# Performance work log

Measured on AMD Instinct MI355X. Metric: run time of the kernel, lower is better.

## Reference

```python
import jax, jax.numpy as jnp
import numpy as np

V, E, H, B, S, T, FF = 50000, 128, 256, 32, 256, 32, 4096
START = 2  # tokenizer.word_index['<start>'] stand-in


def setup_inputs() -> dict:
    key = jax.random.key(0)
    ks = jax.random.split(key, 16)
    g = lambda k, shape, s=0.05: (jax.random.normal(k, shape) * s).astype(jnp.float32)
    z = lambda shape: jnp.zeros(shape, jnp.float32)
    return {
        "inp": jax.random.randint(ks[0], (B, S), 0, V, dtype=jnp.int32),
        "targ": jax.random.randint(ks[1], (B, T), 0, V, dtype=jnp.int32),
        "emb": g(ks[2], (V, E)),
        "ek_f": g(ks[3], (E, 4 * H)), "er_f": g(ks[4], (H, 4 * H)), "eb_f": z((4 * H,)),
        "ek_b": g(ks[5], (E, 4 * H)), "er_b": g(ks[6], (H, 4 * H)), "eb_b": z((4 * H,)),
        "dk": g(ks[7], (E, 4 * H)), "dr": g(ks[8], (H, 4 * H)), "db": z((4 * H,)),
        "henc_w": g(ks[9], (2 * H, E)), "henc_b": z((E,)),
        "sdec_w": g(ks[10], (H, E)), "sdec_b": z((E,)),
        "vatt": g(ks[11], (E, 1)),
        "lf_w": g(ks[12], (2 * H + H, FF), 0.02), "lf_b": z((FF,)),
        "lv_w": g(ks[13], (FF, V), 0.02), "lv_b": z((V,)),
    }


def _lstm_cell(x, h, c, k, rk, b):
    # Keras LSTM gate order: i, f, g(candidate), o
    zg = x @ k + h @ rk + b
    i, f, g, o = jnp.split(zg, 4, axis=-1)
    c = jax.nn.sigmoid(f) * c + jax.nn.sigmoid(i) * jnp.tanh(g)
    h = jax.nn.sigmoid(o) * jnp.tanh(c)
    return h, c


def _run_lstm(xs, k, rk, b):
    # xs: [S, B, E] -> outputs [S, B, H]
    h0 = jnp.zeros((xs.shape[1], rk.shape[0]), xs.dtype)

    def step(carry, x):
        h, c = _lstm_cell(x, carry[0], carry[1], k, rk, b)
        return (h, c), h

    _, hs = jax.lax.scan(step, (h0, h0), xs)
    return hs


def reference(inp, targ, emb, ek_f, er_f, eb_f, ek_b, er_b, eb_b, dk, dr, db,
              henc_w, henc_b, sdec_w, sdec_b, vatt, lf_w, lf_b, lv_w, lv_b):
    # ---- BiLSTM encoder ----
    xs = emb[inp].transpose(1, 0, 2)                       # [S, B, E]
    fwd = _run_lstm(xs, ek_f, er_f, eb_f)                  # [S, B, H]
    bwd = _run_lstm(xs[::-1], ek_b, er_b, eb_b)[::-1]      # [S, B, H]
    enc = jnp.concatenate([fwd, bwd], -1).transpose(1, 0, 2)  # [B, S, 2H]
    henc_proj = enc @ henc_w + henc_b                      # [B, S, E] (loop-invariant)

    # Teacher forcing: step t (t=1..T-1) consumes <start> then targ[:, t-1]
    tok_in = jnp.concatenate(
        [jnp.full((B, 1), START, targ.dtype), targ[:, 1:T - 1]], axis=1)  # [B, T-1]
    tgts = targ[:, 1:]                                     # [B, T-1]
    h0 = jnp.zeros((B, H), jnp.float32)

    def dec_step(carry, tt):
        h, c = carry
        tok, tgt = tt
        h, c = _lstm_cell(emb[tok], h, c, dk, dr, db)
        # Bahdanau attention (note: original uses carry c, not hidden h)
        scores = jnp.tanh(henc_proj + (c @ sdec_w + sdec_b)[:, None, :])  # [B, S, E]
        attn = jax.nn.softmax(scores @ vatt, axis=1)        # [B, S, 1]
        context = jnp.sum(enc * attn, axis=1)               # [B, 2H]
        combined = jnp.concatenate([context, c], axis=1)    # [B, 3H]
        logits = (combined @ lf_w + lf_b) @ lv_w + lv_b     # [B, V]
        logp = jax.nn.log_softmax(logits, axis=-1)
        nll = -jnp.take_along_axis(logp, tgt[:, None].astype(jnp.int32), axis=1)[:, 0]
        mask = (tgt != 0).astype(nll.dtype)
        return (h, c), jnp.mean(nll * mask)

    _, losses = jax.lax.scan(dec_step, (h0, h0), (tok_in.T, tgts.T))
    return jnp.sum(losses) / T
```

## Files before the change

kernel.cpp:

```cpp
#include <hip/hip_runtime.h>

#define DEV __device__ __forceinline__

typedef __attribute__((ext_vector_type(8))) short bf16x8;
typedef __attribute__((ext_vector_type(4))) float f32x4;
typedef __attribute__((ext_vector_type(2))) _Float16 h2_t;

typedef __attribute__((address_space(1))) const void GLDg;
typedef __attribute__((address_space(3))) void GLDl;

static const int V = 50000, E = 128, H = 256, B = 32, S = 256, T = 32, FF = 4096;
static const int NCT = 391;
static const int NPART = 782;
static const size_t OFF_XKF  = 0;
static const size_t OFF_XKB  = 8388608;
static const size_t OFF_XKD  = 16777216;
static const size_t OFF_HSF  = 17825792;
static const size_t OFF_HSB  = 19922944;
static const size_t OFF_HENC = 22020096;
static const size_t OFF_ERPF = 23068672;
static const size_t OFF_ERPB = 23199744;
static const size_t OFF_DRP  = 23330816;
static const size_t OFF_COMB = 23461888;
static const size_t OFF_FB16 = 23855104;
static const size_t OFF_LFWT = 25952256;
static const size_t OFF_LVWT = 27525120;
static const size_t LVWT_FLOATS = 102498304;
static const size_t WS_NEED_BYTES = (OFF_LVWT + LVWT_FLOATS) * 4;
static const size_t OFF_PMAX = 0;
static const size_t OFF_PSUM = 800768;
static const size_t OFF_TLOG = 1601536;
static const size_t OFF_NLL  = 1602560;
static const size_t OFF_CT   = 1603584;

static const size_t ENC_LDS_BYTES = 65536 * 2 + 512 + 4096;

DEV float sigf(float x) { return 1.0f / (1.0f + __expf(-x)); }
DEV float tanh_(float x) {
    x = fminf(fmaxf(x, -20.0f), 20.0f);
    float e = __expf(2.0f * x);
    return (e - 1.0f) / (e + 1.0f);
}
DEV unsigned short f2bf(float f) {
    unsigned int u = __builtin_bit_cast(unsigned int, f);
    u += 0x7FFFu + ((u >> 16) & 1u);
    return (unsigned short)(u >> 16);
}
DEV float bf2f(unsigned short s) {
    unsigned int u = ((unsigned int)s) << 16;
    return __builtin_bit_cast(float, u);
}
DEV float dot2u(unsigned int a, unsigned int b, float c) {
#if __has_builtin(__builtin_amdgcn_fdot2)
    return __builtin_amdgcn_fdot2(__builtin_bit_cast(h2_t, a), __builtin_bit_cast(h2_t, b), c, false);
#else
    h2_t x = __builtin_bit_cast(h2_t, a), y = __builtin_bit_cast(h2_t, b);
    return c + (float)x[0] * (float)y[0] + (float)x[1] * (float)y[1];
#endif
}

__global__ void pack_half_k(const float* __restrict__ erf, const float* __restrict__ erb,
                            const float* __restrict__ dr,
                            unsigned int* __restrict__ pf, unsigned int* __restrict__ pb,
                            unsigned int* __restrict__ pd) {
    int id = blockIdx.x * 256 + threadIdx.x;
    int which = id >> 17;
    int rem = id & 131071;
    const float* s = (which == 0) ? erf : (which == 1) ? erb : dr;
    unsigned int* o = (which == 0) ? pf : (which == 1) ? pb : pd;
    int cc = rem >> 7, k2 = rem & 127;
    float v0 = s[(2 * k2) * 1024 + cc];
    float v1 = s[(2 * k2 + 1) * 1024 + cc];
    h2_t h; h[0] = (_Float16)v0; h[1] = (_Float16)v1;
    o[rem] = __builtin_bit_cast(unsigned int, h);
}

__global__ __launch_bounds__(256) void xgate_kernel(const float* __restrict__ emb,
                                                    const int* __restrict__ tok_src, int dec_mode,
                                                    const float* __restrict__ wt,
                                                    const float* __restrict__ bias,
                                                    float* __restrict__ out) {
    __shared__ float Al[64][128];
    __shared__ int tk[64];
    int r0 = blockIdx.x * 64, c0b = blockIdx.y * 128;
    int tid = threadIdx.x;
    if (tid < 64) {
        int r = r0 + tid; int hi = r >> 5, b = r & 31; int token;
        if (dec_mode) token = (hi == 0) ? 2 : tok_src[b * 32 + hi];
        else          token = tok_src[b * 256 + hi];
        tk[tid] = token;
    }
    __syncthreads();
    {
        int ri = tid >> 2, cc = (tid & 3) * 32;
        const float4* src = (const float4*)&emb[(size_t)tk[ri] * 128 + cc];
        float4* dst = (float4*)&Al[ri][cc];
#pragma unroll
        for (int i = 0; i < 8; ++i) dst[i] = src[i];
    }
    __syncthreads();
    int rg = tid >> 5;
    int c = c0b + (tid & 31) * 4;
    float4 acc[8];
#pragma unroll
    for (int r = 0; r < 8; ++r) acc[r] = make_float4(0.f, 0.f, 0.f, 0.f);
    for (int k = 0; k < 128; k += 4) {
        float4 w0 = *(const float4*)&wt[(k + 0) * 1024 + c];
        float4 w1 = *(const float4*)&wt[(k + 1) * 1024 + c];
        float4 w2 = *(const float4*)&wt[(k + 2) * 1024 + c];
        float4 w3 = *(const float4*)&wt[(k + 3) * 1024 + c];
#pragma unroll
        for (int r = 0; r < 8; ++r) {
            float4 a = *(const float4*)&Al[rg * 8 + r][k];
            acc[r].x += a.x * w0.x + a.y * w1.x + a.z * w2.x + a.w * w3.x;
            acc[r].y += a.x * w0.y + a.y * w1.y + a.z * w2.y + a.w * w3.y;
            acc[r].z += a.x * w0.z + a.y * w1.z + a.z * w2.z + a.w * w3.z;
            acc[r].w += a.x * w0.w + a.y * w1.w + a.z * w2.w + a.w * w3.w;
        }
    }
    float4 b4 = *(const float4*)&bias[c];
#pragma unroll
    for (int r = 0; r < 8; ++r) {
        int row = r0 + rg * 8 + r;
        float4 v = make_float4(acc[r].x + b4.x, acc[r].y + b4.y, acc[r].z + b4.z, acc[r].w + b4.w);
        *(float4*)&out[(size_t)row * 1024 + c] = v;
    }
}

extern __shared__ unsigned char dyn_lds[];
__global__ __launch_bounds__(512)
__attribute__((amdgpu_waves_per_eu(2, 2)))
void lstm_cvt_fused(
        const float* __restrict__ xkf, const float* __restrict__ xkb,
        const unsigned int* __restrict__ erpf, const unsigned int* __restrict__ erpb,
        float* __restrict__ hsf, float* __restrict__ hsb,
        const float* __restrict__ xkd, const unsigned int* __restrict__ drp,
        float* __restrict__ ct_all, unsigned short* __restrict__ comb16,
        const float* __restrict__ lfw, unsigned short* __restrict__ lfwT,
        const float* __restrict__ lvw, unsigned short* __restrict__ lvwT) {
    int bid = blockIdx.x;
    int tid = threadIdx.x;
    if (bid < 96) {
        int is_dec = (bid >= 64);
        int dir = is_dec ? 0 : (bid >> 5);
        int row = is_dec ? (bid - 64) : (bid & 31);
        const float* xk = is_dec ? xkd : (dir ? xkb : xkf);
        const unsigned int* erp = is_dec ? drp : (dir ? erpb : erpf);
        float* hs = dir ? hsb : hsf;
        int nsteps = is_dec ? 31 : 256;
        int ca = 2 * tid;
        uint4* wlA = (uint4*)dyn_lds;
        uint4* wlB = (uint4*)(dyn_lds + 65536);
        unsigned int* h2 = (unsigned int*)(dyn_lds + 131072);
        float* zg = (float*)(dyn_lds + 131072 + 512);

        const uint4* pa = (const uint4*)&erp[(size_t)ca * 128];
        const uint4* pb = (const uint4*)&erp[(size_t)(ca + 1) * 128];
        uint4 wa[24], wb[24];
#pragma unroll
        for (int i = 0; i < 24; ++i) { wa[i] = pa[i]; wb[i] = pb[i]; }
#pragma unroll
        for (int i = 0; i < 24; ++i) {
            asm volatile("" : "+v"(wa[i].x), "+v"(wa[i].y), "+v"(wa[i].z), "+v"(wa[i].w),
                             "+v"(wb[i].x), "+v"(wb[i].y), "+v"(wb[i].z), "+v"(wb[i].w));
        }
#pragma unroll
        for (int j = 0; j < 8; ++j) { wlA[j * 512 + tid] = pa[24 + j]; wlB[j * 512 + tid] = pb[24 + j]; }
        if (tid < 128) h2[tid] = 0u;
        float c_reg = 0.0f;
        __syncthreads();
        int s0 = (!is_dec && dir) ? (nsteps - 1) : 0;
        float2 xcur = *(const float2*)&xk[(size_t)(s0 * 32 + row) * 1024 + ca];
        for (int si = 0; si < nsteps; ++si) {
            int s = (!is_dec && dir) ? (nsteps - 1 - si) : si;
            float2 xnext = make_float2(0.f, 0.f);
            if (si + 1 < nsteps) {
                int sn = (!is_dec && dir) ? (nsteps - 2 - si) : (si + 1);
                xnext = *(const float2*)&xk[(size_t)(sn * 32 + row) * 1024 + ca];
            }
            float acc0 = xcur.x, acc1 = xcur.y;
#pragma unroll
            for (int i = 0; i < 24; ++i) {
                uint4 hv = *(const uint4*)&h2[4 * i];
                acc0 = dot2u(hv.x, wa[i].x, acc0);
                acc0 = dot2u(hv.y, wa[i].y, acc0);
                acc0 = dot2u(hv.z, wa[i].z, acc0);
                acc0 = dot2u(hv.w, wa[i].w, acc0);
                acc1 = dot2u(hv.x, wb[i].x, acc1);
                acc1 = dot2u(hv.y, wb[i].y, acc1);
                acc1 = dot2u(hv.z, wb[i].z, acc1);
                acc1 = dot2u(hv.w, wb[i].w, acc1);
            }
#pragma unroll
            for (int j = 0; j < 8; ++j) {
                uint4 hv = *(const uint4*)&h2[96 + 4 * j];
                uint4 qa = wlA[j * 512 + tid];
                uint4 qb = wlB[j * 512 + tid];
                acc0 = dot2u(hv.x, qa.x, acc0);
                acc0 = dot2u(hv.y, qa.y, acc0);
                acc0 = dot2u(hv.z, qa.z, acc0);
                acc0 = dot2u(hv.w, qa.w, acc0);
                acc1 = dot2u(hv.x, qb.x, acc1);
                acc1 = dot2u(hv.y, qb.y, acc1);
                acc1 = dot2u(hv.z, qb.z, acc1);
                acc1 = dot2u(hv.w, qb.w, acc1);
            }
            *(float2*)&zg[ca] = make_float2(acc0, acc1);
            __syncthreads();
            if (tid < 256) {
                float ii = zg[tid], ff = zg[tid + 256], gg = zg[tid + 512], oo = zg[tid + 768];
                c_reg = sigf(ff) * c_reg + sigf(ii) * tanh_(gg);
                float h = sigf(oo) * tanh_(c_reg);
                ((_Float16*)h2)[tid] = (_Float16)h;
                if (is_dec) {
                    ct_all[(size_t)(s * 32 + row) * 256 + tid] = c_reg;
                    comb16[(size_t)(s * 32 + row) * 768 + 512 + tid] = f2bf(c_reg);
                } else {
                    hs[(size_t)(s * 32 + row) * 256 + tid] = h;
                }
            }
            __syncthreads();
            xcur = xnext;
        }
        if (is_dec) {
            size_t base = (size_t)(31 * 32 + row) * 768;
            for (int j = tid; j < 768; j += 512) comb16[base + j] = 0;
        }
    } else {
        const float* src; unsigned short* dst; int N, ldd, nb, kb, nmax;
        if (bid < 96 + 192) {
            int f2 = bid - 96;
            src = lfw; dst = lfwT; N = 4096; ldd = 768; nmax = 4096;
            nb = (f2 & 15) * 256; kb = (f2 >> 4) * 64;
        } else {
            int f3 = bid - 288;
            src = lvw; dst = lvwT; N = 50000; ldd = 4096; nmax = 50048;
            int nbi = f3 % 196, kbi = f3 / 196;
            nb = nbi * 256; kb = kbi * 64;
        }
        unsigned int* l32 = (unsigned int*)dyn_lds;
        int nl = tid & 63, kg = tid >> 6;
        float4 v[8];
        if (nb + 256 <= N) {
            const float* sp = src + (size_t)(kb + kg * 8) * N + nb + nl * 4;
#pragma unroll
            for (int j = 0; j < 8; ++j) v[j] = *(const float4*)(sp + (size_t)j * N);
        } else {
#pragma unroll
            for (int j = 0; j < 8; ++j) {
                int n0 = nb + nl * 4;
                const float* rp = src + (size_t)(kb + kg * 8 + j) * N;
                v[j].x = (n0 + 0 < N) ? rp[n0 + 0] : 0.0f;
                v[j].y = (n0 + 1 < N) ? rp[n0 + 1] : 0.0f;
                v[j].z = (n0 + 2 < N) ? rp[n0 + 2] : 0.0f;
                v[j].w = (n0 + 3 < N) ? rp[n0 + 3] : 0.0f;
            }
        }
#pragma unroll
        for (int p = 0; p < 4; ++p) {
            unsigned int d0 = (unsigned int)f2bf(v[2 * p].x) | ((unsigned int)f2bf(v[2 * p + 1].x) << 16);
            unsigned int d1 = (unsigned int)f2bf(v[2 * p].y) | ((unsigned int)f2bf(v[2 * p + 1].y) << 16);
            unsigned int d2 = (unsigned int)f2bf(v[2 * p].z) | ((unsigned int)f2bf(v[2 * p + 1].z) << 16);
            unsigned int d3 = (unsigned int)f2bf(v[2 * p].w) | ((unsigned int)f2bf(v[2 * p + 1].w) << 16);
            *(uint4*)&l32[(size_t)(kg * 4 + p) * 260 + nl * 4] = make_uint4(d0, d1, d2, d3);
        }
        __syncthreads();
#pragma unroll
        for (int i = 0; i < 4; ++i) {
            int cid = i * 512 + tid;
            int nloc = cid >> 3, kc = cid & 7;
            int n = nb + nloc;
            if (n < nmax) {
                unsigned int u0 = l32[(size_t)(kc * 4 + 0) * 260 + nloc];
                unsigned int u1 = l32[(size_t)(kc * 4 + 1) * 260 + nloc];
                unsigned int u2 = l32[(size_t)(kc * 4 + 2) * 260 + nloc];
                unsigned int u3 = l32[(size_t)(kc * 4 + 3) * 260 + nloc];
                *(uint4*)&dst[(size_t)n * ldd + kb + kc * 8] = make_uint4(u0, u1, u2, u3);
            }
        }
    }
}

__global__ __launch_bounds__(256) void dec_attn(const float* __restrict__ ct_all,
                                                const float* __restrict__ sdw, const float* __restrict__ sdb,
                                                const float* __restrict__ vatt,
                                                const float* __restrict__ henc,
                                                const float* __restrict__ hsf, const float* __restrict__ hsb,
                                                unsigned short* __restrict__ comb16) {
    int per = (int)gridDim.x >> 3;
    int f = ((int)blockIdx.x & 7) * per + ((int)blockIdx.x >> 3);
    int row = f / 31, t = f - row * 31;
    int tid = threadIdx.x;
    __shared__ float c_l[256];
    __shared__ float catt[128];
    __shared__ float attn[256];
    __shared__ float red[256];
    __shared__ float vat[128];
    __shared__ float part[256];
    c_l[tid] = ct_all[(size_t)(t * 32 + row) * 256 + tid];
    if (tid < 128) vat[tid] = vatt[tid];
    __syncthreads();
    {
        int col = tid & 127, k0 = (tid >> 7) * 128;
        float aa = 0.0f;
#pragma unroll 4
        for (int k = 0; k < 128; ++k) aa += c_l[k0 + k] * sdw[(size_t)(k0 + k) * 128 + col];
        part[tid] = aa;
    }
    __syncthreads();
    if (tid < 128) catt[tid] = part[tid] + part[tid + 128] + sdb[tid];
    __syncthreads();
    {
        const float4* hp = (const float4*)&henc[(size_t)(row * 256 + tid) * 128];
        float aa = 0.0f;
#pragma unroll 4
        for (int e4 = 0; e4 < 32; ++e4) {
            float4 h4 = hp[e4];
            int e = 4 * e4;
            aa += tanh_(h4.x + catt[e + 0]) * vat[e + 0];
            aa += tanh_(h4.y + catt[e + 1]) * vat[e + 1];
            aa += tanh_(h4.z + catt[e + 2]) * vat[e + 2];
            aa += tanh_(h4.w + catt[e + 3]) * vat[e + 3];
        }
        attn[tid] = aa;
    }
    __syncthreads();
    red[tid] = attn[tid];
    __syncthreads();
    for (int off = 128; off; off >>= 1) {
        if (tid < off) red[tid] = fmaxf(red[tid], red[tid + off]);
        __syncthreads();
    }
    float mx = red[0];
    __syncthreads();
    float ex = __expf(attn[tid] - mx);
    red[tid] = ex;
    __syncthreads();
    for (int off = 128; off; off >>= 1) {
        if (tid < off) red[tid] += red[tid + off];
        __syncthreads();
    }
    float inv = 1.0f / red[0];
    __syncthreads();
    attn[tid] = ex * inv;
    __syncthreads();
    {
        float cx0 = 0.0f, cx1 = 0.0f;
#pragma unroll 4
        for (int s = 0; s < 256; ++s) {
            float aw = attn[s];
            cx0 += aw * hsf[(size_t)(s * 32 + row) * 256 + tid];
            cx1 += aw * hsb[(size_t)(s * 32 + row) * 256 + tid];
        }
        size_t base = (size_t)(t * 32 + row) * 768;
        comb16[base + tid] = f2bf(cx0);
        comb16[base + 256 + tid] = f2bf(cx1);
    }
}

__global__ __launch_bounds__(256) void henc_kernel(const float* __restrict__ hsf, const float* __restrict__ hsb,
                                                   const float* __restrict__ hw, const float* __restrict__ hb,
                                                   float* __restrict__ henc) {
    __shared__ float Al[32][256];
    int r0 = blockIdx.x * 32;
    int tid = threadIdx.x;
    int rg = tid >> 5;
    int c = (tid & 31) * 4;
    float4 acc[4];
#pragma unroll
    for (int r = 0; r < 4; ++r) acc[r] = make_float4(0.f, 0.f, 0.f, 0.f);
    for (int kc = 0; kc < 2; ++kc) {
        const float* src_arr = kc ? hsb : hsf;
        {
            int ri = tid >> 3, cc = (tid & 7) * 32;
            int r = r0 + ri; int b = r >> 8, s = r & 255;
            const float4* sp = (const float4*)&src_arr[(size_t)(s * 32 + b) * 256 + cc];
            float4* dp = (float4*)&Al[ri][cc];
#pragma unroll
            for (int i = 0; i < 8; ++i) dp[i] = sp[i];
        }
        __syncthreads();
        for (int k = 0; k < 256; k += 4) {
            int kg = kc * 256 + k;
            float4 w0 = *(const float4*)&hw[(kg + 0) * 128 + c];
            float4 w1 = *(const float4*)&hw[(kg + 1) * 128 + c];
            float4 w2 = *(const float4*)&hw[(kg + 2) * 128 + c];
            float4 w3 = *(const float4*)&hw[(kg + 3) * 128 + c];
#pragma unroll
            for (int r = 0; r < 4; ++r) {
                float4 a = *(const float4*)&Al[rg * 4 + r][k];
                acc[r].x += a.x * w0.x + a.y * w1.x + a.z * w2.x + a.w * w3.x;
                acc[r].y += a.x * w0.y + a.y * w1.y + a.z * w2.y + a.w * w3.y;
                acc[r].z += a.x * w0.z + a.y * w1.z + a.z * w2.z + a.w * w3.z;
                acc[r].w += a.x * w0.w + a.y * w1.w + a.z * w2.w + a.w * w3.w;
            }
        }
        __syncthreads();
    }
    float4 b4 = *(const float4*)&hb[c];
#pragma unroll
    for (int r = 0; r < 4; ++r) {
        int row = r0 + rg * 4 + r;
        float4 v = make_float4(acc[r].x + b4.x, acc[r].y + b4.y, acc[r].z + b4.z, acc[r].w + b4.w);
        *(float4*)&henc[(size_t)row * 128 + c] = v;
    }
}

template <int MODE>
__global__ __launch_bounds__(256, 4) void gemm_bt(const unsigned short* __restrict__ A, int lda, int K,
                                                  const unsigned short* __restrict__ Bt, int ldb, int ncols,
                                                  const float* __restrict__ bias,
                                                  unsigned short* __restrict__ outC,
                                                  float* __restrict__ Pmax, float* __restrict__ Psum, int npart,
                                                  const int* __restrict__ targ, float* __restrict__ tlog) {
    __shared__ unsigned int AL[128 * 16];
    __shared__ unsigned int BL[128 * 16];
    __shared__ int tgt_l[128];
    int per = (int)gridDim.x >> 3;
    int f = ((int)blockIdx.x & 7) * per + ((int)blockIdx.x >> 3);
    int ct = f >> 3, rt = f & 7;
    int tid = threadIdx.x;
    int lane = tid & 63, w = tid >> 6;
    int wr = w >> 1, wc = w & 1;
    if (MODE == 1 && tid < 128) {
        int row = rt * 128 + tid;
        int tt = row >> 5, bb = row & 31;
        tgt_l[tid] = (tt < 31) ? targ[bb * 32 + tt + 1] : -1;
    }
    f32x4 acc[4][4];
#pragma unroll
    for (int i = 0; i < 4; ++i)
#pragma unroll
        for (int j = 0; j < 4; ++j) acc[i][j] = (f32x4){0.f, 0.f, 0.f, 0.f};

    int P0 = tid,       r0 = P0 >> 2, c0 = (P0 & 3) ^ ((r0 >> 1) & 3);
    int P1 = 256 + tid, r1 = P1 >> 2, c1 = (P1 & 3) ^ ((r1 >> 1) & 3);
    const unsigned short* ag0 = A + (size_t)(rt * 128 + r0) * lda + c0 * 8;
    const unsigned short* ag1 = A + (size_t)(rt * 128 + r1) * lda + c1 * 8;
    const unsigned short* bg0 = Bt + (size_t)(ct * 128 + r0) * ldb + c0 * 8;
    const unsigned short* bg1 = Bt + (size_t)(ct * 128 + r1) * ldb + c1 * 8;
    unsigned int* adst0 = &AL[(size_t)(w * 64) * 4];
    unsigned int* adst1 = &AL[(size_t)(256 + w * 64) * 4];
    unsigned int* bdst0 = &BL[(size_t)(w * 64) * 4];
    unsigned int* bdst1 = &BL[(size_t)(256 + w * 64) * 4];

    int iters = K / 32;
    for (int it = 0; it < iters; ++it) {
        size_t k0 = (size_t)it * 32;
        __builtin_amdgcn_global_load_lds((GLDg*)(ag0 + k0), (GLDl*)adst0, 16, 0, 0);
        __builtin_amdgcn_global_load_lds((GLDg*)(ag1 + k0), (GLDl*)adst1, 16, 0, 0);
        __builtin_amdgcn_global_load_lds((GLDg*)(bg0 + k0), (GLDl*)bdst0, 16, 0, 0);
        __builtin_amdgcn_global_load_lds((GLDg*)(bg1 + k0), (GLDl*)bdst1, 16, 0, 0);
        __syncthreads();
        bf16x8 af[4];
#pragma unroll
        for (int i = 0; i < 4; ++i) {
            int r = wr * 64 + i * 16 + (lane & 15);
            int pos = (lane >> 4) ^ ((r >> 1) & 3);
            af[i] = *(const bf16x8*)&AL[r * 16 + pos * 4];
        }
#pragma unroll
        for (int j = 0; j < 4; ++j) {
            int n = wc * 64 + j * 16 + (lane & 15);
            int pos = (lane >> 4) ^ ((n >> 1) & 3);
            bf16x8 bfr = *(const bf16x8*)&BL[n * 16 + pos * 4];
#pragma unroll
            for (int i = 0; i < 4; ++i)
                acc[i][j] = __builtin_amdgcn_mfma_f32_16x16x32_bf16(af[i], bfr, acc[i][j], 0, 0, 0);
        }
        __syncthreads();
    }
    float bv[4]; bool vok[4];
#pragma unroll
    for (int j = 0; j < 4; ++j) {
        int col = ct * 128 + wc * 64 + j * 16 + (lane & 15);
        vok[j] = (col < ncols);
        bv[j] = vok[j] ? bias[col] : 0.0f;
    }
    if (MODE == 0) {
#pragma unroll
        for (int i = 0; i < 4; ++i)
#pragma unroll
            for (int reg = 0; reg < 4; ++reg) {
                int row = rt * 128 + wr * 64 + i * 16 + (lane >> 4) * 4 + reg;
#pragma unroll
                for (int j = 0; j < 4; ++j) {
                    int col = ct * 128 + wc * 64 + j * 16 + (lane & 15);
                    outC[(size_t)row * 4096 + col] = f2bf(acc[i][j][reg] + bv[j]);
                }
            }
    } else {
#pragma unroll
        for (int i = 0; i < 4; ++i)
#pragma unroll
            for (int reg = 0; reg < 4; ++reg) {
                int rowl = wr * 64 + i * 16 + (lane >> 4) * 4 + reg;
                int row = rt * 128 + rowl;
                int ntgt = tgt_l[rowl];
                float v[4];
                float m = -1e30f;
#pragma unroll
                for (int j = 0; j < 4; ++j) {
                    v[j] = vok[j] ? (acc[i][j][reg] + bv[j]) : -1e30f;
                    m = fmaxf(m, v[j]);
                }
#pragma unroll
                for (int j = 0; j < 4; ++j) {
                    int col = ct * 128 + wc * 64 + j * 16 + (lane & 15);
                    if (col == ntgt) tlog[row] = v[j];
                }
                m = fmaxf(m, __shfl_xor(m, 1));
                m = fmaxf(m, __shfl_xor(m, 2));
                m = fmaxf(m, __shfl_xor(m, 4));
                m = fmaxf(m, __shfl_xor(m, 8));
                float s = 0.0f;
#pragma unroll
                for (int j = 0; j < 4; ++j) s += __expf(v[j] - m);
                s += __shfl_xor(s, 1);
                s += __shfl_xor(s, 2);
                s += __shfl_xor(s, 4);
                s += __shfl_xor(s, 8);
                if ((lane & 15) == 0) {
                    Pmax[(size_t)row * npart + ct * 2 + wc] = m;
                    Psum[(size_t)row * npart + ct * 2 + wc] = s;
                }
            }
    }
}

__global__ __launch_bounds__(256, 3) void gemm_big1(const unsigned short* __restrict__ A, int lda, int K,
                                                    const float* __restrict__ Bm, int Nstride,
                                                    const float* __restrict__ bias,
                                                    float* __restrict__ Pmax, float* __restrict__ Psum, int npart,
                                                    const int* __restrict__ targ, float* __restrict__ tlog) {
    __shared__ unsigned int AL[128 * 16];
    __shared__ unsigned int BL[128 * 16];
    __shared__ int tgt_l[128];
    int per = (int)gridDim.x >> 3;
    int f = ((int)blockIdx.x & 7) * per + ((int)blockIdx.x >> 3);
    int ct = f >> 3, rt = f & 7;
    int tid = threadIdx.x;
    int lane = tid & 63, w = tid >> 6;
    int wr = w >> 1, wc = w & 1;
    if (tid < 128) {
        int row = rt * 128 + tid;
        int tt = row >> 5, bb = row & 31;
        tgt_l[tid] = (tt < 31) ? targ[bb * 32 + tt + 1] : -1;
    }
    f32x4 acc[4][4];
#pragma unroll
    for (int i = 0; i < 4; ++i)
#pragma unroll
        for (int j = 0; j < 4; ++j) acc[i][j] = (f32x4){0.f, 0.f, 0.f, 0.f};
    int P0 = tid,       r0 = P0 >> 2, c0 = (P0 & 3) ^ ((r0 >> 1) & 3);
    int P1 = 256 + tid, r1 = P1 >> 2, c1 = (P1 & 3) ^ ((r1 >> 1) & 3);
    const unsigned short* ag0 = A + (size_t)(rt * 128 + r0) * lda + c0 * 8;
    const unsigned short* ag1 = A + (size_t)(rt * 128 + r1) * lda + c1 * 8;
    unsigned int* ldst0 = &AL[(size_t)(w * 64) * 4];
    unsigned int* ldst1 = &AL[(size_t)(256 + w * 64) * 4];
    int bn = tid & 127, bkh = tid >> 7;
    int coln = ct * 128 + bn;
    bool colok = (coln < Nstride);
    const float* bp = Bm + (size_t)(bkh * 16) * Nstride + (colok ? coln : 0);
    int bs = (bn >> 1) & 3;
    unsigned int* bw0 = &BL[bn * 16 + (((bkh * 2) ^ bs) * 4)];
    unsigned int* bw1 = &BL[bn * 16 + (((bkh * 2 + 1) ^ bs) * 4)];
    int iters = K / 32;
    for (int it = 0; it < iters; ++it) {
        size_t k0 = (size_t)it * 32;
        __builtin_amdgcn_global_load_lds((GLDg*)(ag0 + k0), (GLDl*)ldst0, 16, 0, 0);
        __builtin_amdgcn_global_load_lds((GLDg*)(ag1 + k0), (GLDl*)ldst1, 16, 0, 0);
        {
            const float* bq = bp + k0 * Nstride;
            unsigned int dw[8];
#pragma unroll
            for (int i = 0; i < 8; ++i) {
                float f0 = colok ? bq[(size_t)(2 * i) * Nstride] : 0.0f;
                float f1 = colok ? bq[(size_t)(2 * i + 1) * Nstride] : 0.0f;
                dw[i] = (unsigned int)f2bf(f0) | ((unsigned int)f2bf(f1) << 16);
            }
            *(uint4*)bw0 = make_uint4(dw[0], dw[1], dw[2], dw[3]);
            *(uint4*)bw1 = make_uint4(dw[4], dw[5], dw[6], dw[7]);
        }
        __syncthreads();
        bf16x8 af[4];
#pragma unroll
        for (int i = 0; i < 4; ++i) {
            int r = wr * 64 + i * 16 + (lane & 15);
            int pos = (lane >> 4) ^ ((r >> 1) & 3);
            af[i] = *(const bf16x8*)&AL[r * 16 + pos * 4];
        }
#pragma unroll
        for (int j = 0; j < 4; ++j) {
            int n = wc * 64 + j * 16 + (lane & 15);
            int pos = (lane >> 4) ^ ((n >> 1) & 3);
            bf16x8 bfr = *(const bf16x8*)&BL[n * 16 + pos * 4];
#pragma unroll
            for (int i = 0; i < 4; ++i)
                acc[i][j] = __builtin_amdgcn_mfma_f32_16x16x32_bf16(af[i], bfr, acc[i][j], 0, 0, 0);
        }
        __syncthreads();
    }
    float bv[4]; bool vok[4];
#pragma unroll
    for (int j = 0; j < 4; ++j) {
        int col = ct * 128 + wc * 64 + j * 16 + (lane & 15);
        vok[j] = (col < Nstride);
        bv[j] = vok[j] ? bias[col] : 0.0f;
    }
#pragma unroll
    for (int i = 0; i < 4; ++i)
#pragma unroll
        for (int reg = 0; reg < 4; ++reg) {
            int rowl = wr * 64 + i * 16 + (lane >> 4) * 4 + reg;
            int row = rt * 128 + rowl;
            int ntgt = tgt_l[rowl];
            float v[4];
            float m = -1e30f;
#pragma unroll
            for (int j = 0; j < 4; ++j) {
                v[j] = vok[j] ? (acc[i][j][reg] + bv[j]) : -1e30f;
                m = fmaxf(m, v[j]);
            }
#pragma unroll
            for (int j = 0; j < 4; ++j) {
                int col = ct * 128 + wc * 64 + j * 16 + (lane & 15);
                if (col == ntgt) tlog[row] = v[j];
            }
            m = fmaxf(m, __shfl_xor(m, 1));
            m = fmaxf(m, __shfl_xor(m, 2));
            m = fmaxf(m, __shfl_xor(m, 4));
            m = fmaxf(m, __shfl_xor(m, 8));
            float s = 0.0f;
#pragma unroll
            for (int j = 0; j < 4; ++j) s += __expf(v[j] - m);
            s += __shfl_xor(s, 1);
            s += __shfl_xor(s, 2);
            s += __shfl_xor(s, 4);
            s += __shfl_xor(s, 8);
            if ((lane & 15) == 0) {
                Pmax[(size_t)row * npart + ct * 2 + wc] = m;
                Psum[(size_t)row * npart + ct * 2 + wc] = s;
            }
        }
}

__global__ __launch_bounds__(256) void lse_nll(const float* __restrict__ Pmax, const float* __restrict__ Psum,
                                               const float* __restrict__ tlog, const int* __restrict__ targ,
                                               float* __restrict__ nll) {
    int row = blockIdx.x;
    int t = row >> 5, b = row & 31;
    int tid = threadIdx.x;
    __shared__ float rm[256];
    __shared__ float rs[256];
    float m = -1e30f;
    for (int i = tid; i < NPART; i += 256) m = fmaxf(m, Pmax[(size_t)row * NPART + i]);
    rm[tid] = m;
    __syncthreads();
    for (int off = 128; off; off >>= 1) {
        if (tid < off) rm[tid] = fmaxf(rm[tid], rm[tid + off]);
        __syncthreads();
    }
    m = rm[0];
    float s = 0.0f;
    for (int i = tid; i < NPART; i += 256)
        s += Psum[(size_t)row * NPART + i] * __expf(Pmax[(size_t)row * NPART + i] - m);
    rs[tid] = s;
    __syncthreads();
    for (int off = 128; off; off >>= 1) {
        if (tid < off) rs[tid] += rs[tid + off];
        __syncthreads();
    }
    if (tid == 0) {
        float lse = m + logf(rs[0]);
        float out = 0.0f;
        if (t < 31) {
            int tg = targ[b * 32 + t + 1];
            if (tg != 0) out = lse - tlog[row];
        }
        nll[row] = out;
    }
}

__global__ __launch_bounds__(256) void finloss(const float* __restrict__ nll, float* __restrict__ out) {
    __shared__ float red[256];
    int tid = threadIdx.x;
    float a = 0.0f;
    for (int i = tid; i < 1024; i += 256) a += nll[i];
    red[tid] = a;
    __syncthreads();
    for (int off = 128; off; off >>= 1) {
        if (tid < off) red[tid] += red[tid + off];
        __syncthreads();
    }
    if (tid == 0) out[0] = red[0] * (1.0f / 1024.0f);
}

extern "C" void kernel_launch(void* const* d_in, const int* in_sizes, int n_in,
                              void* d_out, int out_size, void* d_ws, size_t ws_size,
                              hipStream_t stream) {
    const int* inp = (const int*)d_in[0];
    const int* targ = (const int*)d_in[1];
    const float* emb = (const float*)d_in[2];
    const float* ekf = (const float*)d_in[3];
    const float* erf = (const float*)d_in[4];
    const float* ebf = (const float*)d_in[5];
    const float* ekb = (const float*)d_in[6];
    const float* erb = (const float*)d_in[7];
    const float* ebb = (const float*)d_in[8];
    const float* dk  = (const float*)d_in[9];
    const float* dr  = (const float*)d_in[10];
    const float* db  = (const float*)d_in[11];
    const float* hw  = (const float*)d_in[12];
    const float* hb  = (const float*)d_in[13];
    const float* sdw = (const float*)d_in[14];
    const float* sdb = (const float*)d_in[15];
    const float* vat = (const float*)d_in[16];
    const float* lfw = (const float*)d_in[17];
    const float* lfb = (const float*)d_in[18];
    const float* lvw = (const float*)d_in[19];
    const float* lvb = (const float*)d_in[20];

    float* ws = (float*)d_ws;
    float* xkf = ws + OFF_XKF;
    float* xkb = ws + OFF_XKB;
    float* xkd = ws + OFF_XKD;
    float* hsf = ws + OFF_HSF;
    float* hsb = ws + OFF_HSB;
    float* henc = ws + OFF_HENC;
    unsigned int* erpf = (unsigned int*)(ws + OFF_ERPF);
    unsigned int* erpb = (unsigned int*)(ws + OFF_ERPB);
    unsigned int* drp  = (unsigned int*)(ws + OFF_DRP);
    unsigned short* comb16 = (unsigned short*)(ws + OFF_COMB);
    unsigned short* fb16   = (unsigned short*)(ws + OFF_FB16);
    unsigned short* lfwT   = (unsigned short*)(ws + OFF_LFWT);
    unsigned short* lvwT   = (unsigned short*)(ws + OFF_LVWT);
    float* pmax = ws + OFF_PMAX;
    float* psum = ws + OFF_PSUM;
    float* tlog = ws + OFF_TLOG;
    float* nllb = ws + OFF_NLL;
    float* ct_all = ws + OFF_CT;

    bool big = (ws_size >= WS_NEED_BYTES);

    static bool attr_set = false;
    if (!attr_set) {
        hipFuncSetAttribute((const void*)lstm_cvt_fused,
                            hipFuncAttributeMaxDynamicSharedMemorySize, (int)ENC_LDS_BYTES);
        attr_set = true;
    }

    hipLaunchKernelGGL(pack_half_k, dim3(1536), dim3(256), 0, stream, erf, erb, dr, erpf, erpb, drp);
    hipLaunchKernelGGL(xgate_kernel, dim3(128, 8), dim3(256), 0, stream, emb, inp, 0, ekf, ebf, xkf);
    hipLaunchKernelGGL(xgate_kernel, dim3(128, 8), dim3(256), 0, stream, emb, inp, 0, ekb, ebb, xkb);
    hipLaunchKernelGGL(xgate_kernel, dim3(16, 8), dim3(256), 0, stream, emb, targ, 1, dk, db, xkd);
    {
        int nblk = big ? (288 + 12544) : 288;
        hipLaunchKernelGGL(lstm_cvt_fused, dim3(nblk), dim3(512), ENC_LDS_BYTES, stream,
                           xkf, xkb, erpf, erpb, hsf, hsb,
                           xkd, drp, ct_all, comb16,
                           lfw, lfwT, lvw, lvwT);
    }
    hipLaunchKernelGGL(henc_kernel, dim3(256), dim3(256), 0, stream, hsf, hsb, hw, hb, henc);
    hipLaunchKernelGGL(dec_attn, dim3(992), dim3(256), 0, stream,
                       ct_all, sdw, sdb, vat, henc, hsf, hsb, comb16);
    hipLaunchKernelGGL((gemm_bt<0>), dim3(256), dim3(256), 0, stream,
                       comb16, 768, 768, lfwT, 768, 4096, lfb, fb16,
                       (float*)nullptr, (float*)nullptr, 0, (const int*)nullptr, (float*)nullptr);
    if (big)
        hipLaunchKernelGGL((gemm_bt<1>), dim3(3128), dim3(256), 0, stream,
                           fb16, 4096, 4096, lvwT, 4096, 50000, lvb, (unsigned short*)nullptr,
                           pmax, psum, NPART, targ, tlog);
    else
        hipLaunchKernelGGL(gemm_big1, dim3(3128), dim3(256), 0, stream,
                           fb16, 4096, 4096, lvw, 50000, lvb, pmax, psum, NPART, targ, tlog);
    hipLaunchKernelGGL(lse_nll, dim3(1024), dim3(256), 0, stream, pmax, psum, tlog, targ, nllb);
    hipLaunchKernelGGL(finloss, dim3(1), dim3(256), 0, stream, nllb, (float*)d_out);
}
```

Before: 2.217 ms.

## Use 1024-thread blocks so each LSTM thread computes a single gate column

The fused recurrence kernel now launches 1024 threads per block. Each thread owns one of the 1024 gate columns, where it previously owned two, which halves the per-step dot-product work per thread and the register-held weights per thread. The weight-conversion blocks sharing the same launch are retiled to cover 128 k-values per block, which halves their block count. The old waves-per-EU attribute is dropped, so under the tighter per-thread register budget of a 1024-thread block the 96-register weight cache may spill.

```diff
diff --git a/kernel.cpp b/kernel.cpp
--- a/kernel.cpp
+++ b/kernel.cpp
@@ -33,7 +33,7 @@
 static const size_t OFF_NLL  = 1602560;
 static const size_t OFF_CT   = 1603584;
 
-static const size_t ENC_LDS_BYTES = 65536 * 2 + 512 + 4096;
+static const size_t ENC_LDS_BYTES = 131072 + 512 + 4096;
 
 DEV float sigf(float x) { return 1.0f / (1.0f + __expf(-x)); }
 DEV float tanh_(float x) {
@@ -128,9 +128,7 @@
 }
 
 extern __shared__ unsigned char dyn_lds[];
-__global__ __launch_bounds__(512)
-__attribute__((amdgpu_waves_per_eu(2, 2)))
-void lstm_cvt_fused(
+__global__ __launch_bounds__(1024) void lstm_cvt_fused(
         const float* __restrict__ xkf, const float* __restrict__ xkb,
         const unsigned int* __restrict__ erpf, const unsigned int* __restrict__ erpb,
         float* __restrict__ hsf, float* __restrict__ hsb,
@@ -148,37 +146,33 @@
         const unsigned int* erp = is_dec ? drp : (dir ? erpb : erpf);
         float* hs = dir ? hsb : hsf;
         int nsteps = is_dec ? 31 : 256;
-        int ca = 2 * tid;
-        uint4* wlA = (uint4*)dyn_lds;
-        uint4* wlB = (uint4*)(dyn_lds + 65536);
+        uint4* wl = (uint4*)dyn_lds;
         unsigned int* h2 = (unsigned int*)(dyn_lds + 131072);
         float* zg = (float*)(dyn_lds + 131072 + 512);
 
-        const uint4* pa = (const uint4*)&erp[(size_t)ca * 128];
-        const uint4* pb = (const uint4*)&erp[(size_t)(ca + 1) * 128];
-        uint4 wa[24], wb[24];
-#pragma unroll
-        for (int i = 0; i < 24; ++i) { wa[i] = pa[i]; wb[i] = pb[i]; }
+        const uint4* pa = (const uint4*)&erp[(size_t)tid * 128];
+        uint4 wa[24];
+#pragma unroll
+        for (int i = 0; i < 24; ++i) wa[i] = pa[i];
 #pragma unroll
         for (int i = 0; i < 24; ++i) {
-            asm volatile("" : "+v"(wa[i].x), "+v"(wa[i].y), "+v"(wa[i].z), "+v"(wa[i].w),
-                             "+v"(wb[i].x), "+v"(wb[i].y), "+v"(wb[i].z), "+v"(wb[i].w));
-        }
-#pragma unroll
-        for (int j = 0; j < 8; ++j) { wlA[j * 512 + tid] = pa[24 + j]; wlB[j * 512 + tid] = pb[24 + j]; }
+            asm volatile("" : "+v"(wa[i].x), "+v"(wa[i].y), "+v"(wa[i].z), "+v"(wa[i].w));
+        }
+#pragma unroll
+        for (int j = 0; j < 8; ++j) wl[j * 1024 + tid] = pa[24 + j];
         if (tid < 128) h2[tid] = 0u;
         float c_reg = 0.0f;
         __syncthreads();
         int s0 = (!is_dec && dir) ? (nsteps - 1) : 0;
-        float2 xcur = *(const float2*)&xk[(size_t)(s0 * 32 + row) * 1024 + ca];
+        float xcur = xk[(size_t)(s0 * 32 + row) * 1024 + tid];
         for (int si = 0; si < nsteps; ++si) {
             int s = (!is_dec && dir) ? (nsteps - 1 - si) : si;
-            float2 xnext = make_float2(0.f, 0.f);
+            float xnext = 0.0f;
             if (si + 1 < nsteps) {
                 int sn = (!is_dec && dir) ? (nsteps - 2 - si) : (si + 1);
-                xnext = *(const float2*)&xk[(size_t)(sn * 32 + row) * 1024 + ca];
-            }
-            float acc0 = xcur.x, acc1 = xcur.y;
+                xnext = xk[(size_t)(sn * 32 + row) * 1024 + tid];
+            }
+            float acc0 = xcur;
 #pragma unroll
             for (int i = 0; i < 24; ++i) {
                 uint4 hv = *(const uint4*)&h2[4 * i];
@@ -186,26 +180,17 @@
                 acc0 = dot2u(hv.y, wa[i].y, acc0);
                 acc0 = dot2u(hv.z, wa[i].z, acc0);
                 acc0 = dot2u(hv.w, wa[i].w, acc0);
-                acc1 = dot2u(hv.x, wb[i].x, acc1);
-                acc1 = dot2u(hv.y, wb[i].y, acc1);
-                acc1 = dot2u(hv.z, wb[i].z, acc1);
-                acc1 = dot2u(hv.w, wb[i].w, acc1);
             }
 #pragma unroll
             for (int j = 0; j < 8; ++j) {
                 uint4 hv = *(const uint4*)&h2[96 + 4 * j];
-                uint4 qa = wlA[j * 512 + tid];
-                uint4 qb = wlB[j * 512 + tid];
+                uint4 qa = wl[j * 1024 + tid];
                 acc0 = dot2u(hv.x, qa.x, acc0);
                 acc0 = dot2u(hv.y, qa.y, acc0);
                 acc0 = dot2u(hv.z, qa.z, acc0);
                 acc0 = dot2u(hv.w, qa.w, acc0);
-                acc1 = dot2u(hv.x, qb.x, acc1);
-                acc1 = dot2u(hv.y, qb.y, acc1);
-                acc1 = dot2u(hv.z, qb.z, acc1);
-                acc1 = dot2u(hv.w, qb.w, acc1);
-            }
-            *(float2*)&zg[ca] = make_float2(acc0, acc1);
+            }
+            zg[tid] = acc0;
             __syncthreads();
             if (tid < 256) {
                 float ii = zg[tid], ff = zg[tid + 256], gg = zg[tid + 512], oo = zg[tid + 768];
@@ -224,19 +209,19 @@
         }
         if (is_dec) {
             size_t base = (size_t)(31 * 32 + row) * 768;
-            for (int j = tid; j < 768; j += 512) comb16[base + j] = 0;
+            for (int j = tid; j < 768; j += 1024) comb16[base + j] = 0;
         }
     } else {
         const float* src; unsigned short* dst; int N, ldd, nb, kb, nmax;
-        if (bid < 96 + 192) {
+        if (bid < 96 + 96) {
             int f2 = bid - 96;
             src = lfw; dst = lfwT; N = 4096; ldd = 768; nmax = 4096;
-            nb = (f2 & 15) * 256; kb = (f2 >> 4) * 64;
+            nb = (f2 & 15) * 256; kb = (f2 >> 4) * 128;
         } else {
-            int f3 = bid - 288;
+            int f3 = bid - 192;
             src = lvw; dst = lvwT; N = 50000; ldd = 4096; nmax = 50048;
             int nbi = f3 % 196, kbi = f3 / 196;
-            nb = nbi * 256; kb = kbi * 64;
+            nb = nbi * 256; kb = kbi * 128;
         }
         unsigned int* l32 = (unsigned int*)dyn_lds;
         int nl = tid & 63, kg = tid >> 6;
@@ -267,8 +252,8 @@
         __syncthreads();
 #pragma unroll
         for (int i = 0; i < 4; ++i) {
-            int cid = i * 512 + tid;
-            int nloc = cid >> 3, kc = cid & 7;
+            int cid = i * 1024 + tid;
+            int nloc = cid >> 4, kc = cid & 15;
             int n = nb + nloc;
             if (n < nmax) {
                 unsigned int u0 = l32[(size_t)(kc * 4 + 0) * 260 + nloc];
@@ -755,8 +740,8 @@
     hipLaunchKernelGGL(xgate_kernel, dim3(128, 8), dim3(256), 0, stream, emb, inp, 0, ekb, ebb, xkb);
     hipLaunchKernelGGL(xgate_kernel, dim3(16, 8), dim3(256), 0, stream, emb, targ, 1, dk, db, xkd);
     {
-        int nblk = big ? (288 + 12544) : 288;
-        hipLaunchKernelGGL(lstm_cvt_fused, dim3(nblk), dim3(512), ENC_LDS_BYTES, stream,
+        int nblk = big ? (192 + 6272) : 192;
+        hipLaunchKernelGGL(lstm_cvt_fused, dim3(nblk), dim3(1024), ENC_LDS_BYTES, stream,
                            xkf, xkb, erpf, erpb, hsf, hsb,
                            xkd, drp, ct_all, comb16,
                            lfw, lfwT, lvw, lvwT);
```

After: 3.162 ms. 42.6% more time.
